# Optimization experiments

Hardware: AMD Instinct MI355X
Metric: run time of the kernel (lower is better)

Reference implementation:

```python
import jax, jax.numpy as jnp
import numpy as np

N_NODES = 100000
N_EDGES = 3200000


def setup_inputs() -> dict:
    key = jax.random.key(0)
    ks = jax.random.split(key, 20)
    x = jax.random.normal(ks[0], (N_NODES, 3), dtype=jnp.float32)
    edge_index = jax.random.randint(ks[1], (2, N_EDGES), 0, N_NODES, dtype=jnp.int64)

    def w(k, shape, fan_in):
        return jax.random.normal(k, shape, dtype=jnp.float32) * (1.0 / np.sqrt(fan_in))

    return {
        "x": x, "edge_index": edge_index,
        # layer 1: in=3, out=16, heads=2
        "W1": w(ks[2], (3, 32), 3), "a_src1": w(ks[3], (2, 16), 16), "a_dst1": w(ks[4], (2, 16), 16), "b1": jnp.zeros((32,), jnp.float32),
        # layer 2: in=32, out=16, heads=2
        "W2": w(ks[5], (32, 32), 32), "a_src2": w(ks[6], (2, 16), 16), "a_dst2": w(ks[7], (2, 16), 16), "b2": jnp.zeros((32,), jnp.float32),
        # layer 3: in=32, out=16, heads=1
        "W3": w(ks[8], (32, 16), 32), "a_src3": w(ks[9], (1, 16), 16), "a_dst3": w(ks[10], (1, 16), 16), "b3": jnp.zeros((16,), jnp.float32),
        # output linear 16 -> 1
        "Wout": w(ks[11], (16, 1), 16), "bout": jnp.zeros((1,), jnp.float32),
    }


def gat_layer(x, src, dst, W, a_src, a_dst, b, heads, ch, n):
    # h: [N, H, C]
    h = (x @ W).reshape(n, heads, ch)
    alpha_src = jnp.sum(h * a_src[None], axis=-1)  # [N, H]
    alpha_dst = jnp.sum(h * a_dst[None], axis=-1)  # [N, H]
    e = jax.nn.leaky_relu(alpha_src[src] + alpha_dst[dst], 0.2)  # [E, H]
    # segment softmax over incoming edges of each dst node
    m = jax.ops.segment_max(e, dst, num_segments=n)
    m = jnp.where(jnp.isfinite(m), m, 0.0)
    ex = jnp.exp(e - jax.lax.stop_gradient(m)[dst])
    s = jax.ops.segment_sum(ex, dst, num_segments=n)
    alpha = ex / (s[dst] + 1e-16)  # [E, H]
    out = jax.ops.segment_sum(h[src] * alpha[:, :, None], dst, num_segments=n)  # [N, H, C]
    return out.reshape(n, heads * ch) + b


def reference(x, edge_index, W1, a_src1, a_dst1, b1, W2, a_src2, a_dst2, b2,
              W3, a_src3, a_dst3, b3, Wout, bout):
    n = x.shape[0]
    loops = jnp.arange(n, dtype=edge_index.dtype)
    src = jnp.concatenate([edge_index[0], loops])  # PyG add_self_loops=True
    dst = jnp.concatenate([edge_index[1], loops])
    h = jax.nn.elu(gat_layer(x, src, dst, W1, a_src1, a_dst1, b1, 2, 16, n))
    h = jax.nn.elu(gat_layer(h, src, dst, W2, a_src2, a_dst2, b2, 2, 16, n))
    h = jax.nn.elu(gat_layer(h, src, dst, W3, a_src3, a_dst3, b3, 1, 16, n))
    embeddings = h
    out = jax.nn.sigmoid(h @ Wout + bout)
    return out, embeddings
```

## Files before the change

kernel.cpp:

```cpp
#include <hip/hip_runtime.h>
#include <hip/hip_fp16.h>
#include <math.h>

#define TPB 256
#define PMAX 128
#define PSH 10
#define PW  1024
#define CHUNK 8192
#define PCAP 49152

__device__ __forceinline__ float leaky02(float x) { return x > 0.f ? x : 0.2f * x; }
__device__ __forceinline__ float eluf(float x) { return x > 0.f ? x : (__expf(x) - 1.f); }


__global__ void zero_kernel(int* __restrict__ p, int n) {
  int i = blockIdx.x * blockDim.x + threadIdx.x;
  if (i < n) p[i] = 0;
}

__global__ __launch_bounds__(256) void scatter_kernel(const int* __restrict__ src,
                                                      const int* __restrict__ dst,
                                                      int E, int n,
                                                      int* __restrict__ pcursor,
                                                      unsigned* __restrict__ pstage) {
  __shared__ int lcnt[PMAX];
  __shared__ int lscan[PMAX];
  __shared__ int lbase[PMAX];
  __shared__ int wtot;
  __shared__ unsigned slab[CHUNK];
  int Etot = E + n;
  int c0 = blockIdx.x * CHUNK;
  if (c0 >= Etot) return;
  int c1 = min(c0 + CHUNK, Etot);
  int m = c1 - c0;
  for (int j = threadIdx.x; j < PMAX; j += TPB) lcnt[j] = 0;
  __syncthreads();
  for (int idx = c0 + threadIdx.x; idx < c1; idx += TPB) {
    int dd = (idx < E) ? dst[idx] : (idx - E);
    atomicAdd(&lcnt[dd >> PSH], 1);
  }
  __syncthreads();
  int myv = 0, myx = 0;
  if (threadIdx.x < PMAX) {
    int lane = threadIdx.x & 63;
    myv = lcnt[threadIdx.x];
    myx = myv;
#pragma unroll
    for (int off = 1; off < 64; off <<= 1) {
      int u = __shfl_up(myx, off);
      if (lane >= off) myx += u;
    }
    if (threadIdx.x == 63) wtot = myx;
  }
  __syncthreads();
  if (threadIdx.x < PMAX) {
    int excl = myx - myv + ((threadIdx.x >= 64) ? wtot : 0);
    lscan[threadIdx.x] = excl;
    lbase[threadIdx.x] = myv ? atomicAdd(&pcursor[threadIdx.x], myv) : 0;
    lcnt[threadIdx.x] = 0;
  }
  __syncthreads();
  for (int idx = c0 + threadIdx.x; idx < c1; idx += TPB) {
    int ss, dd;
    if (idx < E) { ss = src[idx]; dd = dst[idx]; }
    else         { ss = dd = idx - E; }
    int p = dd >> PSH;
    int pos = lscan[p] + atomicAdd(&lcnt[p], 1);
    slab[pos] = ((unsigned)ss << PSH) | (unsigned)(dd & (PW - 1));
  }
  __syncthreads();
  for (int t = threadIdx.x; t < m; t += TPB) {
    int lo = 0, hi = PMAX - 1;
    while (lo < hi) {
      int mid = (lo + hi + 1) >> 1;
      if (lscan[mid] <= t) lo = mid; else hi = mid - 1;
    }
    pstage[(size_t)lo * PCAP + lbase[lo] + (t - lscan[lo])] = slab[t];
  }
}

__global__ __launch_bounds__(PMAX) void pscan_kernel(const int* __restrict__ pcursor,
                                                     int* __restrict__ pbase) {
  __shared__ int ssum[PMAX];
  int t = threadIdx.x;
  int own = pcursor[t];
  ssum[t] = own;
  __syncthreads();
  for (int off = 1; off < PMAX; off <<= 1) {
    int a = (t >= off) ? ssum[t - off] : 0;
    __syncthreads();
    ssum[t] += a;
    __syncthreads();
  }
  pbase[t] = ssum[t] - own;
  if (t == PMAX - 1) pbase[PMAX] = ssum[t];
}

__global__ __launch_bounds__(1024) void build_csr_kernel(const unsigned* __restrict__ pstage,
                                                         const int* __restrict__ pcursor,
                                                         const int* __restrict__ pbase,
                                                         int nvtx,
                                                         int* __restrict__ rowptr,
                                                         int* __restrict__ csr_src) {
  __shared__ int lhist[PW];
  __shared__ int lcur[PW];
  int t = threadIdx.x;
  int lane = t & 63;
  int wid = t >> 6;
  int p = blockIdx.x;
  size_t rbase = (size_t)p * PCAP;
  int cnt = pcursor[p];
  int wbase = pbase[p];
  int nodebase = p << PSH;
  lhist[t] = 0;
  __syncthreads();
  for (int i = t; i < cnt; i += 1024)
    atomicAdd(&lhist[pstage[rbase + i] & (PW - 1)], 1);
  __syncthreads();
  int v = lhist[t];
  int x = v;
#pragma unroll
  for (int off = 1; off < 64; off <<= 1) {
    int u = __shfl_up(x, off);
    if (lane >= off) x += u;
  }
  if (lane == 63) lcur[wid] = x;
  __syncthreads();
  if (t < 16) {
    int wsum = lcur[t];
    int y = wsum;
#pragma unroll
    for (int off = 1; off < 16; off <<= 1) {
      int u = __shfl_up(y, off);
      if (t >= off) y += u;
    }
    lcur[t] = y - wsum;
  }
  __syncthreads();
  int acc = wbase + x + lcur[wid] - v;
  __syncthreads();
  lcur[t] = acc;
  int node = nodebase + t;
  if (node < nvtx) rowptr[node] = acc;
  __syncthreads();
  for (int i = t; i < cnt; i += 1024) {
    unsigned w = pstage[rbase + i];
    int pos = atomicAdd(&lcur[w & (PW - 1)], 1);
    csr_src[pos] = (int)(w >> PSH);
  }
  if (p == (int)gridDim.x - 1 && t == 0) rowptr[nvtx] = wbase + cnt;
}


template<int IN, int OUT, int H>
__global__ void transform_kernel(const float* __restrict__ x, const float* __restrict__ W,
                                 const float* __restrict__ a_src, const float* __restrict__ a_dst,
                                 __half* __restrict__ h, float* __restrict__ asrc,
                                 float* __restrict__ adst, int n) {
  __shared__ float sW[IN * OUT];
  __shared__ float sa[2 * OUT];
  for (int i = threadIdx.x; i < IN * OUT; i += blockDim.x) sW[i] = W[i];
  if (threadIdx.x < OUT) {
    sa[threadIdx.x] = a_src[threadIdx.x];
    sa[OUT + threadIdx.x] = a_dst[threadIdx.x];
  }
  __syncthreads();
  int i = blockIdx.x * blockDim.x + threadIdx.x;
  if (i >= n) return;
  float xv[IN];
#pragma unroll
  for (int k = 0; k < IN; k++) xv[k] = x[(size_t)i * IN + k];
  float hv[OUT];
#pragma unroll
  for (int j = 0; j < OUT; j++) {
    float acc = 0.f;
#pragma unroll
    for (int k = 0; k < IN; k++) acc += xv[k] * sW[k * OUT + j];
    hv[j] = acc;
  }
#pragma unroll
  for (int j = 0; j < OUT; j += 2)
    ((__half2*)h)[((size_t)i * OUT + j) >> 1] = __floats2half2_rn(hv[j], hv[j + 1]);
#pragma unroll
  for (int hh = 0; hh < H; hh++) {
    float as = 0.f, ad = 0.f;
#pragma unroll
    for (int c = 0; c < 16; c++) {
      as += hv[hh * 16 + c] * sa[hh * 16 + c];
      ad += hv[hh * 16 + c] * sa[OUT + hh * 16 + c];
    }
    asrc[i * H + hh] = as;
    adst[i * H + hh] = ad;
  }
}


__global__ __launch_bounds__(256) void node_gat12(
    const int* __restrict__ rowptr,
    const int* __restrict__ csr_src,
    const float* __restrict__ asrc,
    const float* __restrict__ adst,
    const __half* __restrict__ hfeat,
    const float* __restrict__ bias,
    float* __restrict__ outb,
    int n) {
  __shared__ float4 s_e[4][64];
  int wid = threadIdx.x >> 6;
  int lane = threadIdx.x & 63;
  int i = (blockIdx.x * blockDim.x + threadIdx.x) >> 6;
  if (i >= n) return;
  int start = rowptr[i];
  int d = rowptr[i + 1] - start;
  float ad0 = adst[i * 2 + 0];
  float ad1 = adst[i * 2 + 1];
  const uint2* hfp = (const uint2*)hfeat;
  const float2* asrc2 = (const float2*)asrc;
  int g = lane >> 3;
  int q = lane & 7;
  const float2* sp = (const float2*)(&s_e[wid][0]) + (q >> 2);
  float4 acc = make_float4(0.f, 0.f, 0.f, 0.f);
  float sl0 = 0.f, sl1 = 0.f;

  if (d <= 64) {
    int sidx8 = 0;
    float w0 = 0.f, w1 = 0.f;
    if (lane < d) {
      int sidx = csr_src[start + lane];
      sidx8 = sidx << 3;
      float2 av = asrc2[sidx];
      w0 = __expf(leaky02(av.x + ad0));
      w1 = __expf(leaky02(av.y + ad1));
    }
    sl0 = w0; sl1 = w1;
    s_e[wid][lane] = make_float4(__int_as_float(sidx8), w0, __int_as_float(sidx8), w1);
    float2 p[8];
#pragma unroll
    for (int it = 0; it < 8; ++it) p[it] = sp[2 * (g + it * 8)];
    uint2 hv[8];
#pragma unroll
    for (int it = 0; it < 8; ++it) hv[it] = hfp[__float_as_int(p[it].x) + q];
#pragma unroll
    for (int it = 0; it < 8; ++it) {
      float2 fa = __half22float2(*(const __half2*)&hv[it].x);
      float2 fb = __half22float2(*(const __half2*)&hv[it].y);
      float w = p[it].y;
      acc.x += w * fa.x; acc.y += w * fa.y;
      acc.z += w * fb.x; acc.w += w * fb.y;
    }
  } else {
    for (int base = 0; base < d; base += 64) {
      int k = base + lane;
      int sidx8 = 0;
      float w0 = 0.f, w1 = 0.f;
      if (k < d) {
        int sidx = csr_src[start + k];
        sidx8 = sidx << 3;
        float2 av = asrc2[sidx];
        w0 = __expf(leaky02(av.x + ad0));
        w1 = __expf(leaky02(av.y + ad1));
        sl0 += w0; sl1 += w1;
      }
      s_e[wid][lane] = make_float4(__int_as_float(sidx8), w0, __int_as_float(sidx8), w1);
      float2 p[8];
#pragma unroll
      for (int it = 0; it < 8; ++it) p[it] = sp[2 * (g + it * 8)];
      uint2 hv[8];
#pragma unroll
      for (int it = 0; it < 8; ++it) hv[it] = hfp[__float_as_int(p[it].x) + q];
#pragma unroll
      for (int it = 0; it < 8; ++it) {
        float2 fa = __half22float2(*(const __half2*)&hv[it].x);
        float2 fb = __half22float2(*(const __half2*)&hv[it].y);
        float w = p[it].y;
        acc.x += w * fa.x; acc.y += w * fa.y;
        acc.z += w * fb.x; acc.w += w * fb.y;
      }
    }
  }

#pragma unroll
  for (int off = 32; off >= 1; off >>= 1) {
    sl0 += __shfl_xor(sl0, off);
    sl1 += __shfl_xor(sl1, off);
  }
#pragma unroll
  for (int off = 8; off <= 32; off <<= 1) {
    acc.x += __shfl_xor(acc.x, off);
    acc.y += __shfl_xor(acc.y, off);
    acc.z += __shfl_xor(acc.z, off);
    acc.w += __shfl_xor(acc.w, off);
  }
  if (lane < 8) {
    float inv = 1.f / (((lane >= 4) ? sl1 : sl0) + 1e-16f);
    float4 bv = ((const float4*)bias)[lane];
    float4 o;
    o.x = eluf(acc.x * inv + bv.x);
    o.y = eluf(acc.y * inv + bv.y);
    o.z = eluf(acc.z * inv + bv.z);
    o.w = eluf(acc.w * inv + bv.w);
    ((float4*)outb)[(size_t)i * 8 + lane] = o;
  }
}

__global__ __launch_bounds__(256) void node_gat3(
    const int* __restrict__ rowptr,
    const int* __restrict__ csr_src,
    const float* __restrict__ asrc,
    const float* __restrict__ adst,
    const __half* __restrict__ hfeat,
    const float* __restrict__ b3,
    const float* __restrict__ Wout,
    const float* __restrict__ bout,
    float* __restrict__ out,
    int n) {
  __shared__ float2 s_hw[4][64];
  int wid = threadIdx.x >> 6;
  int lane = threadIdx.x & 63;
  int i = (blockIdx.x * blockDim.x + threadIdx.x) >> 6;
  if (i >= n) return;
  int start = rowptr[i];
  int d = rowptr[i + 1] - start;
  float ad0 = adst[i];
  const uint2* hfp = (const uint2*)hfeat;
  int g = lane >> 2;
  int q = lane & 3;
  const float2* sp = s_hw[wid];
  float4 acc = make_float4(0.f, 0.f, 0.f, 0.f);
  float sl = 0.f;

  if (d <= 64) {
    int sidx4 = 0;
    float w0 = 0.f;
    if (lane < d) {
      int sidx = csr_src[start + lane];
      sidx4 = sidx << 2;
      w0 = __expf(leaky02(asrc[sidx] + ad0));
    }
    sl = w0;
    s_hw[wid][lane] = make_float2(__int_as_float(sidx4), w0);
    float2 p[4];
#pragma unroll
    for (int it = 0; it < 4; ++it) p[it] = sp[g + it * 16];
    uint2 hv[4];
#pragma unroll
    for (int it = 0; it < 4; ++it) hv[it] = hfp[__float_as_int(p[it].x) + q];
#pragma unroll
    for (int it = 0; it < 4; ++it) {
      float2 fa = __half22float2(*(const __half2*)&hv[it].x);
      float2 fb = __half22float2(*(const __half2*)&hv[it].y);
      float w = p[it].y;
      acc.x += w * fa.x; acc.y += w * fa.y;
      acc.z += w * fb.x; acc.w += w * fb.y;
    }
  } else {
    for (int base = 0; base < d; base += 64) {
      int k = base + lane;
      int sidx4 = 0;
      float w0 = 0.f;
      if (k < d) {
        int sidx = csr_src[start + k];
        sidx4 = sidx << 2;
        w0 = __expf(leaky02(asrc[sidx] + ad0));
        sl += w0;
      }
      s_hw[wid][lane] = make_float2(__int_as_float(sidx4), w0);
      float2 p[4];
#pragma unroll
      for (int it = 0; it < 4; ++it) p[it] = sp[g + it * 16];
      uint2 hv[4];
#pragma unroll
      for (int it = 0; it < 4; ++it) hv[it] = hfp[__float_as_int(p[it].x) + q];
#pragma unroll
      for (int it = 0; it < 4; ++it) {
        float2 fa = __half22float2(*(const __half2*)&hv[it].x);
        float2 fb = __half22float2(*(const __half2*)&hv[it].y);
        float w = p[it].y;
        acc.x += w * fa.x; acc.y += w * fa.y;
        acc.z += w * fb.x; acc.w += w * fb.y;
      }
    }
  }

#pragma unroll
  for (int off = 32; off >= 1; off >>= 1) sl += __shfl_xor(sl, off);
#pragma unroll
  for (int off = 4; off <= 32; off <<= 1) {
    acc.x += __shfl_xor(acc.x, off);
    acc.y += __shfl_xor(acc.y, off);
    acc.z += __shfl_xor(acc.z, off);
    acc.w += __shfl_xor(acc.w, off);
  }
  float z = 0.f;
  if (lane < 4) {
    float inv = 1.f / (sl + 1e-16f);
    float4 bv = ((const float4*)b3)[lane];
    float4 wv = ((const float4*)Wout)[lane];
    float4 o;
    o.x = eluf(acc.x * inv + bv.x);
    o.y = eluf(acc.y * inv + bv.y);
    o.z = eluf(acc.z * inv + bv.z);
    o.w = eluf(acc.w * inv + bv.w);
    ((float4*)(out + n))[(size_t)i * 4 + lane] = o;
    z = o.x * wv.x + o.y * wv.y + o.z * wv.z + o.w * wv.w;
  }
  z += __shfl_xor(z, 1);
  z += __shfl_xor(z, 2);
  if (lane == 0) out[i] = 1.f / (1.f + __expf(-(z + bout[0])));
}


extern "C" void kernel_launch(void* const* d_in, const int* in_sizes, int n_in,
                              void* d_out, int out_size, void* d_ws, size_t ws_size,
                              hipStream_t stream) {
  const float* x    = (const float*)d_in[0];
  const int*   ei   = (const int*)d_in[1];
  const float* W1   = (const float*)d_in[2];
  const float* as1  = (const float*)d_in[3];
  const float* ad1  = (const float*)d_in[4];
  const float* b1   = (const float*)d_in[5];
  const float* W2   = (const float*)d_in[6];
  const float* as2  = (const float*)d_in[7];
  const float* ad2  = (const float*)d_in[8];
  const float* b2   = (const float*)d_in[9];
  const float* W3   = (const float*)d_in[10];
  const float* as3  = (const float*)d_in[11];
  const float* ad3  = (const float*)d_in[12];
  const float* b3   = (const float*)d_in[13];
  const float* Wout = (const float*)d_in[14];
  const float* bout = (const float*)d_in[15];
  float* out = (float*)d_out;

  const int n = in_sizes[0] / 3;
  const int E = in_sizes[1] / 2;
  const int Etot = E + n;
  const int* src = ei;
  const int* dst = ei + E;
  const int nbC = (Etot + CHUNK - 1) / CHUNK;
  const int NP = ((n - 1) >> PSH) + 1;

  float* ws = (float*)d_ws;
  float* bufH = ws;
  float* bufX = bufH + (size_t)n * 32;
  float* asrc = bufX + (size_t)n * 32;
  float* adst = asrc + (size_t)n * 2;
  int* rowptr  = (int*)(adst + (size_t)n * 2);
  int* pbase   = rowptr + n + 1;
  int* pcursor = pbase + PMAX + 1;
  int* csr_src = pcursor + PMAX;
  unsigned* pstage = (unsigned*)ws;
  __half* hH = (__half*)bufH;

  const int nbN = (n + TPB - 1) / TPB;
  const int nbW = (n + 3) / 4;

  zero_kernel<<<1, PMAX, 0, stream>>>(pcursor, PMAX);
  scatter_kernel<<<nbC, TPB, 0, stream>>>(src, dst, E, n, pcursor, pstage);
  pscan_kernel<<<1, PMAX, 0, stream>>>(pcursor, pbase);
  build_csr_kernel<<<NP, 1024, 0, stream>>>(pstage, pcursor, pbase, n, rowptr, csr_src);

  transform_kernel<3, 32, 2><<<nbN, TPB, 0, stream>>>(x, W1, as1, ad1, hH, asrc, adst, n);
  node_gat12<<<nbW, TPB, 0, stream>>>(rowptr, csr_src, asrc, adst, hH, b1, bufX, n);

  transform_kernel<32, 32, 2><<<nbN, TPB, 0, stream>>>(bufX, W2, as2, ad2, hH, asrc, adst, n);
  node_gat12<<<nbW, TPB, 0, stream>>>(rowptr, csr_src, asrc, adst, hH, b2, bufX, n);

  transform_kernel<32, 16, 1><<<nbN, TPB, 0, stream>>>(bufX, W3, as3, ad3, hH, asrc, adst, n);
  node_gat3<<<nbW, TPB, 0, stream>>>(rowptr, csr_src, asrc, adst, hH, b3, Wout, bout, out, n);
}
```

Measured before the change: 370.0 us.

## Build CSR via global degree count and direct atomic scatter

Replaces the two-pass partition-and-stage CSR build, which binned edges into 128 coarse partitions through shared-memory slabs and a staging buffer, with a classic counting sort. Per-node degrees come from global atomics, a two-level scan produces rowptr, self-loops go in first, and edges are then scattered directly with one global atomic per edge. This removes the staging buffer and the binary-search write-out, but adds 3.2M random global atomics twice and scattered csr_src writes. The neighbour order within a row now depends on atomic timing, so it is no longer deterministic.

```diff
diff --git a/kernel.cpp b/kernel.cpp
--- a/kernel.cpp
+++ b/kernel.cpp
@@ -6,84 +6,70 @@
 #define PMAX 128
 #define PSH 10
 #define PW  1024
-#define CHUNK 8192
-#define PCAP 49152
 
 __device__ __forceinline__ float leaky02(float x) { return x > 0.f ? x : 0.2f * x; }
 __device__ __forceinline__ float eluf(float x) { return x > 0.f ? x : (__expf(x) - 1.f); }
 
 
-__global__ void zero_kernel(int* __restrict__ p, int n) {
+__global__ void init_deg_kernel(int* __restrict__ deg, int n) {
   int i = blockIdx.x * blockDim.x + threadIdx.x;
-  if (i < n) p[i] = 0;
-}
-
-__global__ __launch_bounds__(256) void scatter_kernel(const int* __restrict__ src,
-                                                      const int* __restrict__ dst,
-                                                      int E, int n,
-                                                      int* __restrict__ pcursor,
-                                                      unsigned* __restrict__ pstage) {
-  __shared__ int lcnt[PMAX];
-  __shared__ int lscan[PMAX];
-  __shared__ int lbase[PMAX];
-  __shared__ int wtot;
-  __shared__ unsigned slab[CHUNK];
-  int Etot = E + n;
-  int c0 = blockIdx.x * CHUNK;
-  if (c0 >= Etot) return;
-  int c1 = min(c0 + CHUNK, Etot);
-  int m = c1 - c0;
-  for (int j = threadIdx.x; j < PMAX; j += TPB) lcnt[j] = 0;
+  if (i < n) deg[i] = 1;
+}
+
+__global__ __launch_bounds__(256) void count_deg_kernel(const int* __restrict__ dst, int E,
+                                                        int* __restrict__ deg) {
+  int stride = gridDim.x * blockDim.x;
+  int E4 = E >> 2;
+  const int4* d4 = (const int4*)dst;
+  for (int i = blockIdx.x * blockDim.x + threadIdx.x; i < E4; i += stride) {
+    int4 v = d4[i];
+    atomicAdd(&deg[v.x], 1);
+    atomicAdd(&deg[v.y], 1);
+    atomicAdd(&deg[v.z], 1);
+    atomicAdd(&deg[v.w], 1);
+  }
+  for (int i = (E4 << 2) + blockIdx.x * blockDim.x + threadIdx.x; i < E; i += stride)
+    atomicAdd(&deg[dst[i]], 1);
+}
+
+__global__ __launch_bounds__(1024) void scan_part_kernel(const int* __restrict__ deg, int n,
+                                                         int* __restrict__ rowptr,
+                                                         int* __restrict__ ptot) {
+  __shared__ int lws[16];
+  int t = threadIdx.x;
+  int lane = t & 63;
+  int wid = t >> 6;
+  int node = (blockIdx.x << PSH) + t;
+  int v = (node < n) ? deg[node] : 0;
+  int x = v;
+#pragma unroll
+  for (int off = 1; off < 64; off <<= 1) {
+    int u = __shfl_up(x, off);
+    if (lane >= off) x += u;
+  }
+  if (lane == 63) lws[wid] = x;
   __syncthreads();
-  for (int idx = c0 + threadIdx.x; idx < c1; idx += TPB) {
-    int dd = (idx < E) ? dst[idx] : (idx - E);
-    atomicAdd(&lcnt[dd >> PSH], 1);
+  if (t < 16) {
+    int wsum = lws[t];
+    int y = wsum;
+#pragma unroll
+    for (int off = 1; off < 16; off <<= 1) {
+      int u = __shfl_up(y, off);
+      if (t >= off) y += u;
+    }
+    lws[t] = y - wsum;
   }
   __syncthreads();
-  int myv = 0, myx = 0;
-  if (threadIdx.x < PMAX) {
-    int lane = threadIdx.x & 63;
-    myv = lcnt[threadIdx.x];
-    myx = myv;
-#pragma unroll
-    for (int off = 1; off < 64; off <<= 1) {
-      int u = __shfl_up(myx, off);
-      if (lane >= off) myx += u;
-    }
-    if (threadIdx.x == 63) wtot = myx;
-  }
-  __syncthreads();
-  if (threadIdx.x < PMAX) {
-    int excl = myx - myv + ((threadIdx.x >= 64) ? wtot : 0);
-    lscan[threadIdx.x] = excl;
-    lbase[threadIdx.x] = myv ? atomicAdd(&pcursor[threadIdx.x], myv) : 0;
-    lcnt[threadIdx.x] = 0;
-  }
-  __syncthreads();
-  for (int idx = c0 + threadIdx.x; idx < c1; idx += TPB) {
-    int ss, dd;
-    if (idx < E) { ss = src[idx]; dd = dst[idx]; }
-    else         { ss = dd = idx - E; }
-    int p = dd >> PSH;
-    int pos = lscan[p] + atomicAdd(&lcnt[p], 1);
-    slab[pos] = ((unsigned)ss << PSH) | (unsigned)(dd & (PW - 1));
-  }
-  __syncthreads();
-  for (int t = threadIdx.x; t < m; t += TPB) {
-    int lo = 0, hi = PMAX - 1;
-    while (lo < hi) {
-      int mid = (lo + hi + 1) >> 1;
-      if (lscan[mid] <= t) lo = mid; else hi = mid - 1;
-    }
-    pstage[(size_t)lo * PCAP + lbase[lo] + (t - lscan[lo])] = slab[t];
-  }
-}
-
-__global__ __launch_bounds__(PMAX) void pscan_kernel(const int* __restrict__ pcursor,
+  int excl = x - v + lws[wid];
+  if (node < n) rowptr[node] = excl;
+  if (t == 1023) ptot[blockIdx.x] = excl + v;
+}
+
+__global__ __launch_bounds__(PMAX) void pscan_kernel(const int* __restrict__ ptot, int NP,
                                                      int* __restrict__ pbase) {
   __shared__ int ssum[PMAX];
   int t = threadIdx.x;
-  int own = pcursor[t];
+  int own = (t < NP) ? ptot[t] : 0;
   ssum[t] = own;
   __syncthreads();
   for (int off = 1; off < PMAX; off <<= 1) {
@@ -96,59 +82,41 @@
   if (t == PMAX - 1) pbase[PMAX] = ssum[t];
 }
 
-__global__ __launch_bounds__(1024) void build_csr_kernel(const unsigned* __restrict__ pstage,
-                                                         const int* __restrict__ pcursor,
-                                                         const int* __restrict__ pbase,
-                                                         int nvtx,
-                                                         int* __restrict__ rowptr,
-                                                         int* __restrict__ csr_src) {
-  __shared__ int lhist[PW];
-  __shared__ int lcur[PW];
+__global__ __launch_bounds__(1024) void addback_kernel(int* __restrict__ rowptr,
+                                                       const int* __restrict__ pbase,
+                                                       int n,
+                                                       int* __restrict__ cur,
+                                                       int* __restrict__ csr_src) {
   int t = threadIdx.x;
-  int lane = t & 63;
-  int wid = t >> 6;
-  int p = blockIdx.x;
-  size_t rbase = (size_t)p * PCAP;
-  int cnt = pcursor[p];
-  int wbase = pbase[p];
-  int nodebase = p << PSH;
-  lhist[t] = 0;
-  __syncthreads();
-  for (int i = t; i < cnt; i += 1024)
-    atomicAdd(&lhist[pstage[rbase + i] & (PW - 1)], 1);
-  __syncthreads();
-  int v = lhist[t];
-  int x = v;
-#pragma unroll
-  for (int off = 1; off < 64; off <<= 1) {
-    int u = __shfl_up(x, off);
-    if (lane >= off) x += u;
-  }
-  if (lane == 63) lcur[wid] = x;
-  __syncthreads();
-  if (t < 16) {
-    int wsum = lcur[t];
-    int y = wsum;
-#pragma unroll
-    for (int off = 1; off < 16; off <<= 1) {
-      int u = __shfl_up(y, off);
-      if (t >= off) y += u;
-    }
-    lcur[t] = y - wsum;
-  }
-  __syncthreads();
-  int acc = wbase + x + lcur[wid] - v;
-  __syncthreads();
-  lcur[t] = acc;
-  int node = nodebase + t;
-  if (node < nvtx) rowptr[node] = acc;
-  __syncthreads();
-  for (int i = t; i < cnt; i += 1024) {
-    unsigned w = pstage[rbase + i];
-    int pos = atomicAdd(&lcur[w & (PW - 1)], 1);
-    csr_src[pos] = (int)(w >> PSH);
-  }
-  if (p == (int)gridDim.x - 1 && t == 0) rowptr[nvtx] = wbase + cnt;
+  int node = (blockIdx.x << PSH) + t;
+  if (node < n) {
+    int abs = rowptr[node] + pbase[blockIdx.x];
+    rowptr[node] = abs;
+    cur[node] = abs + 1;
+    csr_src[abs] = node;
+  }
+  if (node == 0) rowptr[n] = pbase[PMAX];
+}
+
+__global__ __launch_bounds__(256) void scatter_direct_kernel(const int* __restrict__ src,
+                                                             const int* __restrict__ dst,
+                                                             int E,
+                                                             int* __restrict__ cur,
+                                                             int* __restrict__ csr_src) {
+  int stride = gridDim.x * blockDim.x;
+  int E4 = E >> 2;
+  const int4* s4 = (const int4*)src;
+  const int4* d4 = (const int4*)dst;
+  for (int i = blockIdx.x * blockDim.x + threadIdx.x; i < E4; i += stride) {
+    int4 s = s4[i];
+    int4 d = d4[i];
+    csr_src[atomicAdd(&cur[d.x], 1)] = s.x;
+    csr_src[atomicAdd(&cur[d.y], 1)] = s.y;
+    csr_src[atomicAdd(&cur[d.z], 1)] = s.z;
+    csr_src[atomicAdd(&cur[d.w], 1)] = s.w;
+  }
+  for (int i = (E4 << 2) + blockIdx.x * blockDim.x + threadIdx.x; i < E; i += stride)
+    csr_src[atomicAdd(&cur[dst[i]], 1)] = src[i];
 }
 
 
@@ -435,7 +403,6 @@
   const int Etot = E + n;
   const int* src = ei;
   const int* dst = ei + E;
-  const int nbC = (Etot + CHUNK - 1) / CHUNK;
   const int NP = ((n - 1) >> PSH) + 1;
 
   float* ws = (float*)d_ws;
@@ -445,18 +412,22 @@
   float* adst = asrc + (size_t)n * 2;
   int* rowptr  = (int*)(adst + (size_t)n * 2);
   int* pbase   = rowptr + n + 1;
-  int* pcursor = pbase + PMAX + 1;
-  int* csr_src = pcursor + PMAX;
-  unsigned* pstage = (unsigned*)ws;
+  int* ptot    = pbase + PMAX + 1;
+  int* csr_src = ptot + PMAX;
+  int* deg = (int*)bufX;
+  int* cur = deg + n;
   __half* hH = (__half*)bufH;
 
   const int nbN = (n + TPB - 1) / TPB;
   const int nbW = (n + 3) / 4;
-
-  zero_kernel<<<1, PMAX, 0, stream>>>(pcursor, PMAX);
-  scatter_kernel<<<nbC, TPB, 0, stream>>>(src, dst, E, n, pcursor, pstage);
-  pscan_kernel<<<1, PMAX, 0, stream>>>(pcursor, pbase);
-  build_csr_kernel<<<NP, 1024, 0, stream>>>(pstage, pcursor, pbase, n, rowptr, csr_src);
+  const int GS = 2048;
+
+  init_deg_kernel<<<nbN, TPB, 0, stream>>>(deg, n);
+  count_deg_kernel<<<GS, TPB, 0, stream>>>(dst, E, deg);
+  scan_part_kernel<<<NP, 1024, 0, stream>>>(deg, n, rowptr, ptot);
+  pscan_kernel<<<1, PMAX, 0, stream>>>(ptot, NP, pbase);
+  addback_kernel<<<NP, 1024, 0, stream>>>(rowptr, pbase, n, cur, csr_src);
+  scatter_direct_kernel<<<GS, TPB, 0, stream>>>(src, dst, E, cur, csr_src);
 
   transform_kernel<3, 32, 2><<<nbN, TPB, 0, stream>>>(x, W1, as1, ad1, hH, asrc, adst, n);
   node_gat12<<<nbW, TPB, 0, stream>>>(rowptr, csr_src, asrc, adst, hH, b1, bufX, n);
```

Measured after the change: 654.6 us. +76.9%, slower.

## Use per-wave partition histograms and smaller chunks in edge scatter kernel

Applied to the files above, without the earlier changes.

The scatter kernel now keeps a separate shared-memory histogram for each wavefront, which cuts LDS atomic contention, and derives each wave's sub-offsets from prefix sums of those counts. The final copy from the slab to global staging is done one partition per wave with lanes striding, replacing the per-element binary search. The chunk size drops from 8192 to 2048, giving four times as many blocks and less LDS per block, at the cost of more global cursor atomics and shorter contiguous write runs per partition.

```diff
diff --git a/kernel.cpp b/kernel.cpp
--- a/kernel.cpp
+++ b/kernel.cpp
@@ -6,7 +6,7 @@
 #define PMAX 128
 #define PSH 10
 #define PW  1024
-#define CHUNK 8192
+#define CHUNK 2048
 #define PCAP 49152
 
 __device__ __forceinline__ float leaky02(float x) { return x > 0.f ? x : 0.2f * x; }
@@ -23,59 +23,61 @@
                                                       int E, int n,
                                                       int* __restrict__ pcursor,
                                                       unsigned* __restrict__ pstage) {
-  __shared__ int lcnt[PMAX];
+  __shared__ int lcnt[4][PMAX];
+  __shared__ int ltot[PMAX];
   __shared__ int lscan[PMAX];
   __shared__ int lbase[PMAX];
   __shared__ int wtot;
   __shared__ unsigned slab[CHUNK];
+  int t = threadIdx.x;
+  int wid = t >> 6;
+  int lane = t & 63;
   int Etot = E + n;
   int c0 = blockIdx.x * CHUNK;
   if (c0 >= Etot) return;
   int c1 = min(c0 + CHUNK, Etot);
-  int m = c1 - c0;
-  for (int j = threadIdx.x; j < PMAX; j += TPB) lcnt[j] = 0;
-  __syncthreads();
-  for (int idx = c0 + threadIdx.x; idx < c1; idx += TPB) {
+  for (int j = t; j < 4 * PMAX; j += TPB) ((int*)lcnt)[j] = 0;
+  __syncthreads();
+  for (int idx = c0 + t; idx < c1; idx += TPB) {
     int dd = (idx < E) ? dst[idx] : (idx - E);
-    atomicAdd(&lcnt[dd >> PSH], 1);
-  }
-  __syncthreads();
-  int myv = 0, myx = 0;
-  if (threadIdx.x < PMAX) {
-    int lane = threadIdx.x & 63;
-    myv = lcnt[threadIdx.x];
-    myx = myv;
+    atomicAdd(&lcnt[wid][dd >> PSH], 1);
+  }
+  __syncthreads();
+  int tot = 0, x = 0;
+  if (t < PMAX) {
+    int a0 = lcnt[0][t], a1 = lcnt[1][t], a2 = lcnt[2][t], a3 = lcnt[3][t];
+    tot = a0 + a1 + a2 + a3;
+    ltot[t] = tot;
+    lcnt[0][t] = 0; lcnt[1][t] = a0; lcnt[2][t] = a0 + a1; lcnt[3][t] = a0 + a1 + a2;
+    x = tot;
 #pragma unroll
     for (int off = 1; off < 64; off <<= 1) {
-      int u = __shfl_up(myx, off);
-      if (lane >= off) myx += u;
-    }
-    if (threadIdx.x == 63) wtot = myx;
-  }
-  __syncthreads();
-  if (threadIdx.x < PMAX) {
-    int excl = myx - myv + ((threadIdx.x >= 64) ? wtot : 0);
-    lscan[threadIdx.x] = excl;
-    lbase[threadIdx.x] = myv ? atomicAdd(&pcursor[threadIdx.x], myv) : 0;
-    lcnt[threadIdx.x] = 0;
-  }
-  __syncthreads();
-  for (int idx = c0 + threadIdx.x; idx < c1; idx += TPB) {
+      int u = __shfl_up(x, off);
+      if (lane >= off) x += u;
+    }
+    if (t == 63) wtot = x;
+  }
+  __syncthreads();
+  if (t < PMAX) {
+    lscan[t] = x - tot + ((t >= 64) ? wtot : 0);
+    lbase[t] = tot ? atomicAdd(&pcursor[t], tot) : 0;
+  }
+  __syncthreads();
+  for (int idx = c0 + t; idx < c1; idx += TPB) {
     int ss, dd;
     if (idx < E) { ss = src[idx]; dd = dst[idx]; }
     else         { ss = dd = idx - E; }
     int p = dd >> PSH;
-    int pos = lscan[p] + atomicAdd(&lcnt[p], 1);
-    slab[pos] = ((unsigned)ss << PSH) | (unsigned)(dd & (PW - 1));
-  }
-  __syncthreads();
-  for (int t = threadIdx.x; t < m; t += TPB) {
-    int lo = 0, hi = PMAX - 1;
-    while (lo < hi) {
-      int mid = (lo + hi + 1) >> 1;
-      if (lscan[mid] <= t) lo = mid; else hi = mid - 1;
-    }
-    pstage[(size_t)lo * PCAP + lbase[lo] + (t - lscan[lo])] = slab[t];
+    int sub = atomicAdd(&lcnt[wid][p], 1);
+    slab[lscan[p] + sub] = ((unsigned)ss << PSH) | (unsigned)(dd & (PW - 1));
+  }
+  __syncthreads();
+  for (int p = wid; p < PMAX; p += 4) {
+    int cnt = ltot[p];
+    int s = lscan[p];
+    size_t b = (size_t)p * PCAP + lbase[p];
+    for (int j = lane; j < cnt; j += 64)
+      pstage[b + j] = slab[s + j];
   }
 }
 
```

New measurement: 378.0 us. 2.1% more time.
